# Kernel tuning notes

Hardware: AMD Instinct MI355X
Metric: run time of the kernel (lower is better)

The kernel has to match this reference:

```python
import jax, jax.numpy as jnp
import numpy as np
from jax.ops import segment_sum

N_NODES = 50000
N_EDGES = 800000
D_IN, D_HID, D_OUT = 128, 128, 64


def setup_inputs() -> dict:
    key = jax.random.key(0)
    ks = jax.random.split(key, 7)
    return {
        "src": jax.random.randint(ks[0], (N_EDGES,), 0, N_NODES, dtype=jnp.int32),
        "dst": jax.random.randint(ks[1], (N_EDGES,), 0, N_NODES, dtype=jnp.int32),
        "x": jax.random.normal(ks[2], (N_NODES, D_IN), dtype=jnp.float32),
        "W1": jax.random.normal(ks[3], (D_IN, D_HID), dtype=jnp.float32) * (1.0 / np.sqrt(D_IN)),
        "b1": jnp.zeros((D_HID,), dtype=jnp.float32),
        "W2": jax.random.normal(ks[4], (D_HID, D_OUT), dtype=jnp.float32) * (1.0 / np.sqrt(D_HID)),
        "b2": jnp.zeros((D_OUT,), dtype=jnp.float32),
    }


def _gcn_layer(src, dst, x, W, b, inv_sqrt_out, inv_sqrt_in):
    # DGL GraphConv, norm='both': h = D_in^{-1/2} A D_out^{-1/2} (x W) + b
    h = (x * inv_sqrt_out[:, None]) @ W          # transform first (in >= out)
    msg = h[src]                                  # gather source messages [E, d]
    agg = segment_sum(msg, dst, num_segments=x.shape[0])
    return agg * inv_sqrt_in[:, None] + b


def reference(src, dst, x, W1, b1, W2, b2):
    n = x.shape[0]
    ones = jnp.ones((src.shape[0],), dtype=x.dtype)
    deg_out = jnp.clip(segment_sum(ones, src, num_segments=n), 1.0)
    deg_in = jnp.clip(segment_sum(ones, dst, num_segments=n), 1.0)
    inv_sqrt_out = jax.lax.rsqrt(deg_out)
    inv_sqrt_in = jax.lax.rsqrt(deg_in)
    h = _gcn_layer(src, dst, x, W1, b1, inv_sqrt_out, inv_sqrt_in)
    h = jax.nn.relu(h)
    h = _gcn_layer(src, dst, h, W2, b2, inv_sqrt_out, inv_sqrt_in)
    return h
```

## Files before the change

kernel.cpp:

```cpp
#include <hip/hip_runtime.h>
#include <hip/hip_fp16.h>

#define D_IN  128
#define D_HID 128
#define D_OUT 64
#define NBMAX 512
#define CHUNK 2048
#define BM 128
#define BK 32

__launch_bounds__(256)
__global__ void k_bucket(const int* __restrict__ src, const int* __restrict__ dst,
                         int E, int NB, int cap,
                         int* __restrict__ cntD, int* __restrict__ cntS,
                         unsigned int* __restrict__ storeD, unsigned char* __restrict__ storeS) {
    __shared__ int lcD[NBMAX], lcS[NBMAX];
    __shared__ int lbD[NBMAX], lbS[NBMAX];
    const int t = threadIdx.x;
    const int e0 = blockIdx.x * CHUNK;
    const int e1 = min(e0 + CHUNK, E);

    for (int i = t; i < NB; i += 256) { lcD[i] = 0; lcS[i] = 0; }
    __syncthreads();
    for (int i = e0 + t; i < e1; i += 256) {
        atomicAdd(&lcD[dst[i] >> 7], 1);
        atomicAdd(&lcS[src[i] >> 7], 1);
    }
    __syncthreads();
    for (int i = t; i < NB; i += 256) {
        lbD[i] = lcD[i] ? atomicAdd(&cntD[i], lcD[i]) : 0;
        lbS[i] = lcS[i] ? atomicAdd(&cntS[i], lcS[i]) : 0;
        lcD[i] = 0; lcS[i] = 0;
    }
    __syncthreads();
    for (int i = e0 + t; i < e1; i += 256) {
        const int s = src[i], d = dst[i];
        const int bd = d >> 7;
        const int pd = lbD[bd] + atomicAdd(&lcD[bd], 1);
        storeD[(long long)bd * cap + pd] = (unsigned int)s | ((unsigned int)(d & 127) << 16);
        const int bs = s >> 7;
        const int ps = lbS[bs] + atomicAdd(&lcS[bs], 1);
        storeS[(long long)bs * cap + ps] = (unsigned char)(s & 127);
    }
}

__launch_bounds__(512)
__global__ void k_scan512(const int* __restrict__ cntD, int* __restrict__ coarse_off,
                          int NB, int* __restrict__ rowptr_last, int E) {
    __shared__ int sh[512];
    const int t = threadIdx.x;
    const int v = (t < NB) ? cntD[t] : 0;
    sh[t] = v; __syncthreads();
    int inc = v;
    for (int off = 1; off < 512; off <<= 1) {
        int o = (t >= off) ? sh[t - off] : 0;
        __syncthreads();
        inc += o; sh[t] = inc;
        __syncthreads();
    }
    if (t < NB) coarse_off[t] = inc - v;
    if (t == 0) *rowptr_last = E;
}

__launch_bounds__(256)
__global__ void k_fin(const unsigned int* __restrict__ storeD, const unsigned char* __restrict__ storeS,
                      const int* __restrict__ cntD, const int* __restrict__ cntS,
                      const int* __restrict__ coarse_off, int cap, int N,
                      int* __restrict__ rowptr, float* __restrict__ inv_in,
                      float* __restrict__ inv_out, unsigned short* __restrict__ csr_src) {
    __shared__ int fh[128];
    __shared__ int sc[128];
    __shared__ int cur[128];
    const int b = blockIdx.x, t = threadIdx.x;
    const long long sb = (long long)b * cap;

    const int cnt  = cntD[b];
    const int base = coarse_off[b];
    if (t < 128) fh[t] = 0;
    __syncthreads();
    for (int i = t; i < cnt; i += 256) atomicAdd(&fh[storeD[sb + i] >> 16], 1);
    __syncthreads();
    if (t < 128) sc[t] = fh[t];
    __syncthreads();
    int inc = (t < 128) ? sc[t] : 0;
    for (int off = 1; off < 128; off <<= 1) {
        int o = (t >= off && t < 128) ? sc[t - off] : 0;
        __syncthreads();
        if (t < 128) { inc += o; sc[t] = inc; }
        __syncthreads();
    }
    if (t < 128) {
        const int excl = inc - fh[t];
        cur[t] = excl;
        const int node = (b << 7) + t;
        if (node < N) {
            rowptr[node] = base + excl;
            inv_in[node] = rsqrtf((float)max(fh[t], 1));
        }
    }
    __syncthreads();
    for (int i = t; i < cnt; i += 256) {
        const unsigned int e = storeD[sb + i];
        const int pos = atomicAdd(&cur[e >> 16], 1);
        csr_src[base + pos] = (unsigned short)(e & 0xFFFFu);
    }

    __syncthreads();
    if (t < 128) fh[t] = 0;
    __syncthreads();
    const int cnts = cntS[b];
    for (int i = t; i < cnts; i += 256) atomicAdd(&fh[storeS[sb + i]], 1);
    __syncthreads();
    if (t < 128) {
        const int node = (b << 7) + t;
        if (node < N) inv_out[node] = rsqrtf((float)max(fh[t], 1));
    }
}

template<int LDN>
__launch_bounds__(256)
__global__ void k_gemm3(const float* __restrict__ X, const float* __restrict__ W,
                        const float* __restrict__ scale, __half* __restrict__ Y, int N) {
    __shared__ float As[BK][BM + 4];
    __shared__ float Bs[BK][64];

    const int t  = threadIdx.x;
    const int tx = t & 15;
    const int ty = t >> 4;
    const int row0 = blockIdx.x * BM;
    const int col0 = blockIdx.y * 64;

    const int xr = t >> 3;
    const int xc = (t & 7) * 4;

    float acc[8][4];
#pragma unroll
    for (int m = 0; m < 8; ++m)
#pragma unroll
        for (int n = 0; n < 4; ++n) acc[m][n] = 0.0f;

    for (int kk = 0; kk < D_IN; kk += BK) {
        __syncthreads();
#pragma unroll
        for (int p = 0; p < 4; ++p) {
            const int r  = p * 32 + xr;
            const int gr = row0 + r;
            float4 v = make_float4(0.f, 0.f, 0.f, 0.f);
            if (gr < N) {
                v = *(const float4*)(X + (long long)gr * D_IN + kk + xc);
                if (scale) { const float s = scale[gr]; v.x *= s; v.y *= s; v.z *= s; v.w *= s; }
            }
            As[xc + 0][r] = v.x;
            As[xc + 1][r] = v.y;
            As[xc + 2][r] = v.z;
            As[xc + 3][r] = v.w;
        }
#pragma unroll
        for (int p = 0; p < 2; ++p) {
            const int flat = p * 256 + t;
            const int kr = flat >> 4;
            const int jc = (flat & 15) * 4;
            *(float4*)&Bs[kr][jc] = *(const float4*)(W + (long long)(kk + kr) * LDN + col0 + jc);
        }
        __syncthreads();

#pragma unroll
        for (int k = 0; k < BK; ++k) {
            const float4 a0 = *(const float4*)&As[k][ty * 8];
            const float4 a1 = *(const float4*)&As[k][ty * 8 + 4];
            const float4 b0 = *(const float4*)&Bs[k][tx * 4];
            const float am[8] = {a0.x, a0.y, a0.z, a0.w, a1.x, a1.y, a1.z, a1.w};
            const float bn[4] = {b0.x, b0.y, b0.z, b0.w};
#pragma unroll
            for (int m = 0; m < 8; ++m)
#pragma unroll
                for (int n = 0; n < 4; ++n)
                    acc[m][n] += am[m] * bn[n];
        }
    }

#pragma unroll
    for (int m = 0; m < 8; ++m) {
        const int gr = row0 + ty * 8 + m;
        if (gr < N) {
            __half2 h0 = __float22half2_rn(make_float2(acc[m][0], acc[m][1]));
            __half2 h1 = __float22half2_rn(make_float2(acc[m][2], acc[m][3]));
            uint2 pk;
            pk.x = *(unsigned int*)&h0;
            pk.y = *(unsigned int*)&h1;
            *(uint2*)(Y + (long long)gr * LDN + col0 + tx * 4) = pk;
        }
    }
}

template<int D, bool RELU>
__launch_bounds__(256)
__global__ void k_gather(const int* __restrict__ rowptr, const unsigned short* __restrict__ csr_src,
                         const __half* __restrict__ Y, const float* __restrict__ inv_in,
                         const float* __restrict__ inv_out, const float* __restrict__ b,
                         float* __restrict__ out, int N) {
    const int wid  = (int)((blockIdx.x * 256u + threadIdx.x) >> 6);
    const int lane = threadIdx.x & 63;
    if (wid >= N) return;

    const int start = rowptr[wid];
    const int end   = rowptr[wid + 1];

    constexpr int LPE = D / 8;
    constexpr int EPW = 64 / LPE;
    const int grp  = lane / LPE;
    const int colh = (lane % LPE) * 8;

    float a[8];
#pragma unroll
    for (int u = 0; u < 8; ++u) a[u] = 0.0f;

    for (int k = start; k < end; k += 64) {
        const int idx = k + lane;
        const int sv  = (idx < end) ? (int)csr_src[idx] : 0;
        const int cnt = min(64, end - k);
        for (int j = 0; j < cnt; j += EPW) {
            const int jj = j + grp;
            const int s  = __shfl(sv, jj);
            if (jj < cnt) {
                const uint4 raw = *(const uint4*)(Y + (long long)s * D + colh);
                const __half2* h = (const __half2*)&raw;
#pragma unroll
                for (int u = 0; u < 4; ++u) {
                    const float2 f = __half22float2(h[u]);
                    a[2 * u]     += f.x;
                    a[2 * u + 1] += f.y;
                }
            }
        }
    }

#pragma unroll
    for (int u = 0; u < 8; ++u) a[u] += __shfl_down(a[u], 32);
#pragma unroll
    for (int u = 0; u < 8; ++u) a[u] += __shfl_down(a[u], 16);
    if (EPW == 8) {
#pragma unroll
        for (int u = 0; u < 8; ++u) a[u] += __shfl_down(a[u], 8);
    }

    if (lane < LPE) {
        const float ii = inv_in[wid];
        const float io = RELU ? inv_out[wid] : 0.0f;
        const float4 b0 = *(const float4*)(b + colh);
        const float4 b1 = *(const float4*)(b + colh + 4);
        float r[8];
        r[0] = a[0] * ii + b0.x; r[1] = a[1] * ii + b0.y;
        r[2] = a[2] * ii + b0.z; r[3] = a[3] * ii + b0.w;
        r[4] = a[4] * ii + b1.x; r[5] = a[5] * ii + b1.y;
        r[6] = a[6] * ii + b1.z; r[7] = a[7] * ii + b1.w;
        if (RELU) {
#pragma unroll
            for (int u = 0; u < 8; ++u) r[u] = fmaxf(r[u], 0.0f) * io;
        }
        float* o = out + (long long)wid * D + colh;
        *(float4*)(o)     = make_float4(r[0], r[1], r[2], r[3]);
        *(float4*)(o + 4) = make_float4(r[4], r[5], r[6], r[7]);
    }
}

extern "C" void kernel_launch(void* const* d_in, const int* in_sizes, int n_in,
                              void* d_out, int out_size, void* d_ws, size_t ws_size,
                              hipStream_t stream) {
    const int*   src = (const int*)d_in[0];
    const int*   dst = (const int*)d_in[1];
    const float* x   = (const float*)d_in[2];
    const float* W1  = (const float*)d_in[3];
    const float* b1  = (const float*)d_in[4];
    const float* W2  = (const float*)d_in[5];
    const float* b2  = (const float*)d_in[6];
    float* out = (float*)d_out;

    const int E  = in_sizes[0];
    const int N  = in_sizes[2] / D_IN;
    const int NB = (N + 127) >> 7;
    const int mean = E / NB;
    const int cap  = mean + mean / 4 + 128;

    char* ws = (char*)d_ws;
    size_t off = 0;
    auto alloc = [&](size_t bytes) -> void* {
        void* p = ws + off;
        off += (bytes + 255) & ~(size_t)255;
        return p;
    };
    float*          inv_out = (float*)alloc((size_t)N * 4);
    float*          inv_in  = (float*)alloc((size_t)N * 4);
    int*            rowptr  = (int*)alloc((size_t)(N + 1) * 4);
    int*            cntD    = (int*)alloc((size_t)NB * 4);
    int*            cntS    = (int*)alloc((size_t)NB * 4);
    int*            coarse  = (int*)alloc((size_t)NB * 4);
    unsigned int*   storeD  = (unsigned int*)alloc((size_t)NB * cap * 4);
    unsigned char*  storeS  = (unsigned char*)alloc((size_t)NB * cap);
    unsigned short* csr_src = (unsigned short*)alloc((size_t)E * 2);
    __half*         Y1      = (__half*)alloc((size_t)N * D_HID * 2);
    float*          H       = (float*)alloc((size_t)N * D_HID * 4);
    __half*         Y2      = (__half*)alloc((size_t)N * D_OUT * 2);
    (void)ws_size; (void)n_in; (void)out_size;

    hipMemsetAsync(cntD, 0, (size_t)NB * 4, stream);
    hipMemsetAsync(cntS, 0, (size_t)NB * 4, stream);

    k_bucket<<<(E + CHUNK - 1) / CHUNK, 256, 0, stream>>>(src, dst, E, NB, cap, cntD, cntS, storeD, storeS);
    k_scan512<<<1, 512, 0, stream>>>(cntD, coarse, NB, rowptr + N, E);
    k_fin<<<NB, 256, 0, stream>>>(storeD, storeS, cntD, cntS, coarse, cap, N,
                                  rowptr, inv_in, inv_out, csr_src);

    {
        dim3 g((N + BM - 1) / BM, D_HID / 64);
        k_gemm3<D_HID><<<g, 256, 0, stream>>>(x, W1, inv_out, Y1, N);
    }
    k_gather<D_HID, true><<<(N + 3) / 4, 256, 0, stream>>>(rowptr, csr_src, Y1, inv_in, inv_out, b1, H, N);

    {
        dim3 g((N + BM - 1) / BM, D_OUT / 64);
        k_gemm3<D_OUT><<<g, 256, 0, stream>>>(H, W2, nullptr, Y2, N);
    }
    k_gather<D_OUT, false><<<(N + 3) / 4, 256, 0, stream>>>(rowptr, csr_src, Y2, inv_in, nullptr, b2, out, N);
}
```

Baseline: 153.9 us.

## Fold coarse scan into finalize, cache bucket edges in LDS, unroll gather loads

Drops the single-block scan kernel: each finalize block computes its own base offset with a block reduction over earlier bucket counts. The two memsets become one tiny zeroing kernel, and rowptr[N] is written by the last finalize block. Finalize stages each bucket's packed edges in a 12KB shared cache, so the second pass does not re-read global memory. The gather loop issues four independent row loads per step to raise memory-level parallelism. In exchange, every finalize block redundantly re-reads up to 391 counts, and the larger shared allocation may lower occupancy.

New measurement: 144.0 us. 6.5% less time.

```diff
diff --git a/kernel.cpp b/kernel.cpp
--- a/kernel.cpp
+++ b/kernel.cpp
@@ -8,6 +8,12 @@
 #define CHUNK 2048
 #define BM 128
 #define BK 32
+#define FCACHE 3072
+
+__global__ void k_zero(int* __restrict__ cntD, int* __restrict__ cntS, int NB) {
+    const int t = threadIdx.x;
+    if (t < NB) { cntD[t] = 0; cntS[t] = 0; }
+}
 
 __launch_bounds__(256)
 __global__ void k_bucket(const int* __restrict__ src, const int* __restrict__ dst,
@@ -44,41 +50,42 @@
     }
 }
 
-__launch_bounds__(512)
-__global__ void k_scan512(const int* __restrict__ cntD, int* __restrict__ coarse_off,
-                          int NB, int* __restrict__ rowptr_last, int E) {
-    __shared__ int sh[512];
-    const int t = threadIdx.x;
-    const int v = (t < NB) ? cntD[t] : 0;
-    sh[t] = v; __syncthreads();
-    int inc = v;
-    for (int off = 1; off < 512; off <<= 1) {
-        int o = (t >= off) ? sh[t - off] : 0;
-        __syncthreads();
-        inc += o; sh[t] = inc;
-        __syncthreads();
-    }
-    if (t < NB) coarse_off[t] = inc - v;
-    if (t == 0) *rowptr_last = E;
-}
-
 __launch_bounds__(256)
 __global__ void k_fin(const unsigned int* __restrict__ storeD, const unsigned char* __restrict__ storeS,
                       const int* __restrict__ cntD, const int* __restrict__ cntS,
-                      const int* __restrict__ coarse_off, int cap, int N,
+                      int cap, int N, int NB, int E,
                       int* __restrict__ rowptr, float* __restrict__ inv_in,
                       float* __restrict__ inv_out, unsigned short* __restrict__ csr_src) {
     __shared__ int fh[128];
     __shared__ int sc[128];
     __shared__ int cur[128];
+    __shared__ int red[256];
+    __shared__ unsigned int ecache[FCACHE];
     const int b = blockIdx.x, t = threadIdx.x;
     const long long sb = (long long)b * cap;
 
-    const int cnt  = cntD[b];
-    const int base = coarse_off[b];
+    int partial = 0;
+    for (int i = t; i < b; i += 256) partial += cntD[i];
+    red[t] = partial;
+    __syncthreads();
+    for (int off = 128; off > 0; off >>= 1) {
+        if (t < off) red[t] += red[t + off];
+        __syncthreads();
+    }
+    const int base = red[0];
+
+    const int cnt = cntD[b];
+    const bool cached = (cnt <= FCACHE);
+    if (cached) {
+        for (int i = t; i < cnt; i += 256) ecache[i] = storeD[sb + i];
+    }
+
     if (t < 128) fh[t] = 0;
     __syncthreads();
-    for (int i = t; i < cnt; i += 256) atomicAdd(&fh[storeD[sb + i] >> 16], 1);
+    for (int i = t; i < cnt; i += 256) {
+        const unsigned int e = cached ? ecache[i] : storeD[sb + i];
+        atomicAdd(&fh[e >> 16], 1);
+    }
     __syncthreads();
     if (t < 128) sc[t] = fh[t];
     __syncthreads();
@@ -98,9 +105,10 @@
             inv_in[node] = rsqrtf((float)max(fh[t], 1));
         }
     }
+    if (b == NB - 1 && t == 128) rowptr[N] = E;
     __syncthreads();
     for (int i = t; i < cnt; i += 256) {
-        const unsigned int e = storeD[sb + i];
+        const unsigned int e = cached ? ecache[i] : storeD[sb + i];
         const int pos = atomicAdd(&cur[e >> 16], 1);
         csr_src[base + pos] = (unsigned short)(e & 0xFFFFu);
     }
@@ -215,22 +223,38 @@
 #pragma unroll
     for (int u = 0; u < 8; ++u) a[u] = 0.0f;
 
+    auto accum = [&](uint4 raw) {
+        const __half2* h = (const __half2*)&raw;
+#pragma unroll
+        for (int u = 0; u < 4; ++u) {
+            const float2 f = __half22float2(h[u]);
+            a[2 * u]     += f.x;
+            a[2 * u + 1] += f.y;
+        }
+    };
+
     for (int k = start; k < end; k += 64) {
         const int idx = k + lane;
         const int sv  = (idx < end) ? (int)csr_src[idx] : 0;
         const int cnt = min(64, end - k);
-        for (int j = 0; j < cnt; j += EPW) {
+        int j = 0;
+        for (; j + 4 * EPW <= cnt; j += 4 * EPW) {
+            const int s0 = __shfl(sv, j + grp);
+            const int s1 = __shfl(sv, j + EPW + grp);
+            const int s2 = __shfl(sv, j + 2 * EPW + grp);
+            const int s3 = __shfl(sv, j + 3 * EPW + grp);
+            const uint4 r0 = *(const uint4*)(Y + (long long)s0 * D + colh);
+            const uint4 r1 = *(const uint4*)(Y + (long long)s1 * D + colh);
+            const uint4 r2 = *(const uint4*)(Y + (long long)s2 * D + colh);
+            const uint4 r3 = *(const uint4*)(Y + (long long)s3 * D + colh);
+            accum(r0); accum(r1); accum(r2); accum(r3);
+        }
+        for (; j < cnt; j += EPW) {
             const int jj = j + grp;
             const int s  = __shfl(sv, jj);
             if (jj < cnt) {
-                const uint4 raw = *(const uint4*)(Y + (long long)s * D + colh);
-                const __half2* h = (const __half2*)&raw;
-#pragma unroll
-                for (int u = 0; u < 4; ++u) {
-                    const float2 f = __half22float2(h[u]);
-                    a[2 * u]     += f.x;
-                    a[2 * u + 1] += f.y;
-                }
+                const uint4 r = *(const uint4*)(Y + (long long)s * D + colh);
+                accum(r);
             }
         }
     }
@@ -294,7 +318,6 @@
     int*            rowptr  = (int*)alloc((size_t)(N + 1) * 4);
     int*            cntD    = (int*)alloc((size_t)NB * 4);
     int*            cntS    = (int*)alloc((size_t)NB * 4);
-    int*            coarse  = (int*)alloc((size_t)NB * 4);
     unsigned int*   storeD  = (unsigned int*)alloc((size_t)NB * cap * 4);
     unsigned char*  storeS  = (unsigned char*)alloc((size_t)NB * cap);
     unsigned short* csr_src = (unsigned short*)alloc((size_t)E * 2);
@@ -303,12 +326,9 @@
     __half*         Y2      = (__half*)alloc((size_t)N * D_OUT * 2);
     (void)ws_size; (void)n_in; (void)out_size;
 
-    hipMemsetAsync(cntD, 0, (size_t)NB * 4, stream);
-    hipMemsetAsync(cntS, 0, (size_t)NB * 4, stream);
-
+    k_zero<<<1, 512, 0, stream>>>(cntD, cntS, NB);
     k_bucket<<<(E + CHUNK - 1) / CHUNK, 256, 0, stream>>>(src, dst, E, NB, cap, cntD, cntS, storeD, storeS);
-    k_scan512<<<1, 512, 0, stream>>>(cntD, coarse, NB, rowptr + N, E);
-    k_fin<<<NB, 256, 0, stream>>>(storeD, storeS, cntD, cntS, coarse, cap, N,
+    k_fin<<<NB, 256, 0, stream>>>(storeD, storeS, cntD, cntS, cap, N, NB, E,
                                   rowptr, inv_in, inv_out, csr_src);
 
     {
```
